# Kernel optimization log

Hardware: AMD Instinct MI355X
Metric: run time of the kernel (lower is better)

Reference implementation:

```python
import jax, jax.numpy as jnp
import numpy as np

C = 1024      # embed dim
NH = 16       # heads
HD = C // NH  # head dim = 64
WS = 14       # window size
MLP_H = 4096  # mlp hidden = 4*C
B, H, W = 16, 28, 28  # batch, token grid (448/16)


def setup_inputs() -> dict:
    key = jax.random.key(0)
    ks = jax.random.split(key, 16)
    s = 0.02
    p = {}
    p["x"] = jax.random.normal(ks[0], (B, H, W, C), jnp.float32)
    p["ln1_w"] = jnp.ones((C,), jnp.float32)
    p["ln1_b"] = jnp.zeros((C,), jnp.float32)
    p["qkv_w"] = jax.random.normal(ks[1], (3 * C, C), jnp.float32) * s
    p["qkv_b"] = jnp.zeros((3 * C,), jnp.float32)
    p["proj_w"] = jax.random.normal(ks[2], (C, C), jnp.float32) * s
    p["proj_b"] = jnp.zeros((C,), jnp.float32)
    p["rel_pos_h"] = jax.random.normal(ks[3], (2 * WS - 1, HD), jnp.float32) * s
    p["rel_pos_w"] = jax.random.normal(ks[4], (2 * WS - 1, HD), jnp.float32) * s
    p["ln2_w"] = jnp.ones((C,), jnp.float32)
    p["ln2_b"] = jnp.zeros((C,), jnp.float32)
    p["fc1_w"] = jax.random.normal(ks[5], (MLP_H, C), jnp.float32) * s
    p["fc1_b"] = jnp.zeros((MLP_H,), jnp.float32)
    p["fc2_w"] = jax.random.normal(ks[6], (C, MLP_H), jnp.float32) * s
    p["fc2_b"] = jnp.zeros((C,), jnp.float32)
    p["conv1_w"] = jax.random.normal(ks[7], (C // 2, C, 1, 1), jnp.float32) * s
    p["n1_w"] = jnp.ones((C // 2,), jnp.float32)
    p["n1_b"] = jnp.zeros((C // 2,), jnp.float32)
    p["conv2_w"] = jax.random.normal(ks[8], (C // 2, C // 2, 3, 3), jnp.float32) * s
    p["n2_w"] = jnp.ones((C // 2,), jnp.float32)
    p["n2_b"] = jnp.zeros((C // 2,), jnp.float32)
    p["conv3_w"] = jax.random.normal(ks[9], (C, C // 2, 1, 1), jnp.float32) * s
    p["n3_w"] = jax.random.normal(ks[10], (C,), jnp.float32) * s
    p["n3_b"] = jnp.zeros((C,), jnp.float32)
    return p


def _ln(x, w, b, eps=1e-5):
    m = x.mean(-1, keepdims=True)
    v = ((x - m) ** 2).mean(-1, keepdims=True)
    return (x - m) * jax.lax.rsqrt(v + eps) * w + b


def _ln_ch(x, w, b, eps=1e-6):
    # detectron2 LayerNorm over channel dim of NCHW
    m = x.mean(1, keepdims=True)
    v = ((x - m) ** 2).mean(1, keepdims=True)
    return (x - m) * jax.lax.rsqrt(v + eps) * w[None, :, None, None] + b[None, :, None, None]


def _win_part(x):
    # [B,H,W,C] -> [B*(H/WS)*(W/WS), WS, WS, C]; 28 is divisible by 14 so no padding
    Bn = x.shape[0]
    x = x.reshape(Bn, H // WS, WS, W // WS, WS, C).transpose(0, 1, 3, 2, 4, 5)
    return x.reshape(-1, WS, WS, C)


def _win_unpart(xw):
    x = xw.reshape(-1, H // WS, W // WS, WS, WS, C).transpose(0, 1, 3, 2, 4, 5)
    return x.reshape(-1, H, W, C)


def _attention(xw, qkv_w, qkv_b, proj_w, proj_b, rel_pos_h, rel_pos_w):
    Bw = xw.shape[0]
    N = WS * WS
    qkv = xw.reshape(Bw, N, C) @ qkv_w.T + qkv_b                       # [Bw,N,3C]
    qkv = qkv.reshape(Bw, N, 3, NH, HD).transpose(2, 3, 0, 1, 4)      # [3,NH,Bw,N,HD]
    q, k, v = qkv.reshape(3, NH * Bw, N, HD)
    attn = (q * HD ** -0.5) @ k.transpose(0, 2, 1)                    # [NH*Bw,N,N]
    # decomposed relative position bias (q_size == k_size == WS)
    idx = jnp.arange(WS)[:, None] - jnp.arange(WS)[None, :] + (WS - 1)
    Rh = rel_pos_h[idx]                                               # [WS,WS,HD]
    Rw = rel_pos_w[idx]
    rq = q.reshape(-1, WS, WS, HD)
    rel_h = jnp.einsum("bhwc,hkc->bhwk", rq, Rh)
    rel_w = jnp.einsum("bhwc,wkc->bhwk", rq, Rw)
    attn = attn.reshape(-1, WS, WS, WS, WS) + rel_h[..., :, None] + rel_w[..., None, :]
    attn = jax.nn.softmax(attn.reshape(NH * Bw, N, N), axis=-1)
    out = attn @ v                                                    # [NH*Bw,N,HD]
    out = out.reshape(NH, Bw, WS, WS, HD).transpose(1, 2, 3, 0, 4).reshape(Bw, WS, WS, C)
    return out @ proj_w.T + proj_b


DN = ("NCHW", "OIHW", "NCHW")


def reference(x, ln1_w, ln1_b, qkv_w, qkv_b, proj_w, proj_b, rel_pos_h, rel_pos_w,
              ln2_w, ln2_b, fc1_w, fc1_b, fc2_w, fc2_b,
              conv1_w, n1_w, n1_b, conv2_w, n2_w, n2_b, conv3_w, n3_w, n3_b):
    shortcut = x
    h = _ln(x, ln1_w, ln1_b)
    h = _win_unpart(_attention(_win_part(h), qkv_w, qkv_b, proj_w, proj_b, rel_pos_h, rel_pos_w))
    x = shortcut + h
    h = _ln(x, ln2_w, ln2_b)
    h = jax.nn.gelu(h @ fc1_w.T + fc1_b, approximate=False)
    x = x + (h @ fc2_w.T + fc2_b)
    # ResBottleneckBlock in NCHW
    y = x.transpose(0, 3, 1, 2)
    r = jax.lax.conv_general_dilated(y, conv1_w, (1, 1), "VALID", dimension_numbers=DN)
    r = jax.nn.gelu(_ln_ch(r, n1_w, n1_b), approximate=False)
    r = jax.lax.conv_general_dilated(r, conv2_w, (1, 1), [(1, 1), (1, 1)], dimension_numbers=DN)
    r = jax.nn.gelu(_ln_ch(r, n2_w, n2_b), approximate=False)
    r = jax.lax.conv_general_dilated(r, conv3_w, (1, 1), "VALID", dimension_numbers=DN)
    r = _ln_ch(r, n3_w, n3_b)
    y = y + r
    return y.transpose(0, 2, 3, 1)
```

## Files before the change

### kernel.cpp

```cpp
#include <hip/hip_runtime.h>
#include <stdint.h>

typedef unsigned short u16;
typedef __attribute__((ext_vector_type(4))) unsigned short u16x4;
typedef __attribute__((ext_vector_type(8))) unsigned short u16x8;
typedef __attribute__((ext_vector_type(8))) __bf16 bf16x8;
typedef __attribute__((ext_vector_type(4))) float f32x4;
typedef __attribute__((ext_vector_type(4))) unsigned int u32x4;

#define TOK 12544
#define CEMB 1024

__device__ __forceinline__ float bf2f(u16 u) {
  union { unsigned int i; float f; } x; x.i = ((unsigned int)u) << 16; return x.f;
}
__device__ __forceinline__ u16 f2bf(float f) {
  union { float f; unsigned int i; } x; x.f = f;
  unsigned int u = x.i;
  u += 0x7fffu + ((u >> 16) & 1u);
  return (u16)(u >> 16);
}
__device__ __forceinline__ float gelu_f(float x) {
  return 0.5f * x * (1.0f + erff(x * 0.7071067811865476f));
}
__device__ __forceinline__ f32x4 mfma_bf16(bf16x8 a, bf16x8 b, f32x4 c) {
  return __builtin_amdgcn_mfma_f32_16x16x32_bf16(a, b, c, 0, 0, 0);
}
__device__ __forceinline__ void glds16(const void* g, void* l) {
  __builtin_amdgcn_global_load_lds(
      (const __attribute__((address_space(1))) void*)g,
      (__attribute__((address_space(3))) void*)l, 16, 0, 0);
}

__global__ __launch_bounds__(256) void zero_k(u32x4* __restrict__ p) {
  u32x4 z = {0u, 0u, 0u, 0u};
  p[threadIdx.x] = z;
}

__global__ __launch_bounds__(256) void cast_bf16_k(const float* __restrict__ in,
                                                   u16* __restrict__ out, int n) {
  int i = (blockIdx.x * 256 + threadIdx.x) * 4;
  if (i >= n) return;
  float4 v = *(const float4*)(in + i);
  u16x4 o = { f2bf(v.x), f2bf(v.y), f2bf(v.z), f2bf(v.w) };
  *(u16x4*)(out + i) = o;
}

__global__ __launch_bounds__(256) void permute_c2_k(const float* __restrict__ in,
                                                    u16* __restrict__ out) {
  int idx = blockIdx.x * 256 + threadIdx.x;
  int o = idx / 4608;
  int rr = idx - o * 4608;
  int pos = rr >> 9;
  int c = rr & 511;
  out[idx] = f2bf(in[(o * 512 + c) * 9 + pos]);
}

template<int COLS, int MODE>
__global__ __launch_bounds__(256)
void ln_k(const float* __restrict__ in, const float* __restrict__ w,
          const float* __restrict__ b, const float* __restrict__ resid,
          u16* __restrict__ outb, float* __restrict__ outf, float eps) {
  int wave = threadIdx.x >> 6, l = threadIdx.x & 63;
  int row = blockIdx.x * 4 + wave;
  const float* x = in + (size_t)row * COLS;
  constexpr int NC = COLS / 256;
  float4 v[NC];
  float s = 0.f, ss = 0.f;
#pragma unroll
  for (int c = 0; c < NC; ++c) {
    v[c] = *(const float4*)(x + (c * 64 + l) * 4);
    s  += v[c].x + v[c].y + v[c].z + v[c].w;
    ss += v[c].x * v[c].x + v[c].y * v[c].y + v[c].z * v[c].z + v[c].w * v[c].w;
  }
#pragma unroll
  for (int off = 32; off; off >>= 1) {
    s  += __shfl_xor(s, off, 64);
    ss += __shfl_xor(ss, off, 64);
  }
  float mean = s * (1.f / COLS);
  float var = ss * (1.f / COLS) - mean * mean;
  float rs = rsqrtf(var + eps);
#pragma unroll
  for (int c = 0; c < NC; ++c) {
    int col = (c * 64 + l) * 4;
    float4 wv = *(const float4*)(w + col);
    float4 bv = *(const float4*)(b + col);
    float o0 = (v[c].x - mean) * rs * wv.x + bv.x;
    float o1 = (v[c].y - mean) * rs * wv.y + bv.y;
    float o2 = (v[c].z - mean) * rs * wv.z + bv.z;
    float o3 = (v[c].w - mean) * rs * wv.w + bv.w;
    if constexpr (MODE == 0) {
      u16x4 o = { f2bf(o0), f2bf(o1), f2bf(o2), f2bf(o3) };
      *(u16x4*)(outb + (size_t)row * COLS + col) = o;
    } else if constexpr (MODE == 1) {
      u16x4 o = { f2bf(gelu_f(o0)), f2bf(gelu_f(o1)), f2bf(gelu_f(o2)), f2bf(gelu_f(o3)) };
      *(u16x4*)(outb + (size_t)row * COLS + col) = o;
    } else {
      float4 rv = *(const float4*)(resid + (size_t)row * COLS + col);
      float4 ov = { rv.x + o0, rv.y + o1, rv.z + o2, rv.w + o3 };
      *(float4*)(outf + (size_t)row * COLS + col) = ov;
    }
  }
}

template<int EPI, bool GATHER>
__global__ __launch_bounds__(256)
void gemm_k(const u16* __restrict__ A, const u16* __restrict__ B,
            int M, int N, int K,
            const float* __restrict__ bias, const float* __restrict__ resid,
            float* __restrict__ outf, u16* __restrict__ outb,
            u16* __restrict__ qg, u16* __restrict__ kg, u16* __restrict__ vg,
            const u16* __restrict__ zeros) {
  __shared__ u16 As[128 * 64];
  __shared__ u16 Bs[128 * 64];
  const int tid = (int)threadIdx.x;
  const int l = tid & 63;
  const int g = l >> 4, r = l & 15;
  const int w = tid >> 6;
  const int wr = w >> 1, wc = w & 1;
  const int rowBase = (int)blockIdx.y * 128;
  const int colBase = (int)blockIdx.x * 128;
  f32x4 acc[4][4] = {};
  const int nk = K >> 6;
  for (int kt = 0; kt < nk; ++kt) {
    __syncthreads();
#pragma unroll
    for (int i = 0; i < 4; ++i) {
      int idx = i * 256 + tid;
      int trow = idx >> 3, tch = idx & 7;
      int tchs = tch ^ (trow & 7);
      const u16* ga;
      if constexpr (!GATHER) {
        ga = A + (size_t)(rowBase + trow) * K + (kt << 6) + (tchs << 3);
      } else {
        int pos = kt >> 3;
        int dy = pos / 3, dx = pos - dy * 3;
        int p = rowBase + trow;
        int bb = p / 784; int rem = p - bb * 784;
        int y = rem / 28; int xx = rem - y * 28;
        int sy = y + dy - 1, sx = xx + dx - 1;
        bool ok = ((unsigned)sy < 28u) && ((unsigned)sx < 28u);
        ga = ok ? (A + (size_t)(bb * 784 + sy * 28 + sx) * 512 + ((kt & 7) << 6) + (tchs << 3))
                : zeros;
      }
      glds16(ga, &As[idx * 8]);
      const u16* gb = B + (size_t)(colBase + trow) * K + (kt << 6) + (tchs << 3);
      glds16(gb, &Bs[idx * 8]);
    }
    __syncthreads();
    bf16x8 af[4][2], bfr[4][2];
#pragma unroll
    for (int m = 0; m < 4; ++m) {
      int rowA = wr * 64 + m * 16 + r;
      int sA = rowA & 7;
      af[m][0] = *(const bf16x8*)&As[rowA * 64 + ((g ^ sA) << 3)];
      af[m][1] = *(const bf16x8*)&As[rowA * 64 + (((g + 4) ^ sA) << 3)];
    }
#pragma unroll
    for (int n = 0; n < 4; ++n) {
      int rowB = wc * 64 + n * 16 + r;
      int sB = rowB & 7;
      bfr[n][0] = *(const bf16x8*)&Bs[rowB * 64 + ((g ^ sB) << 3)];
      bfr[n][1] = *(const bf16x8*)&Bs[rowB * 64 + (((g + 4) ^ sB) << 3)];
    }
#pragma unroll
    for (int m = 0; m < 4; ++m)
#pragma unroll
      for (int n = 0; n < 4; ++n) {
        acc[m][n] = mfma_bf16(af[m][0], bfr[n][0], acc[m][n]);
        acc[m][n] = mfma_bf16(af[m][1], bfr[n][1], acc[m][n]);
      }
  }
#pragma unroll
  for (int m = 0; m < 4; ++m) {
#pragma unroll
    for (int i = 0; i < 4; ++i) {
      int row = rowBase + wr * 64 + m * 16 + g * 4 + i;
#pragma unroll
      for (int n = 0; n < 4; ++n) {
        int col = colBase + wc * 64 + n * 16 + r;
        float v = acc[m][n][i];
        if constexpr (EPI == 0) {
          v += bias[col];
          int bb = row / 784; int rem = row - bb * 784;
          int y = rem / 28; int xx = rem - y * 28;
          int win = bb * 4 + (y / 14) * 2 + (xx / 14);
          int qrow = (y % 14) * 14 + (xx % 14);
          int which = col >> 10; int cid = col & 1023;
          int head = cid >> 6; int d = cid & 63;
          int wh = win * 16 + head;
          u16 bv = f2bf(v);
          if (which == 0)      qg[((size_t)wh * 196 + qrow) * 64 + d] = bv;
          else if (which == 1) kg[((size_t)wh * 196 + qrow) * 64 + d] = bv;
          else                 vg[((size_t)wh * 64 + d) * 224 + qrow] = bv;
        } else if constexpr (EPI == 1) {
          v += bias[col] + resid[(size_t)row * N + col];
          outf[(size_t)row * N + col] = v;
        } else if constexpr (EPI == 2) {
          v = gelu_f(v + bias[col]);
          outb[(size_t)row * N + col] = f2bf(v);
        } else if constexpr (EPI == 3) {
          v += bias[col] + resid[(size_t)row * N + col];
          outf[(size_t)row * N + col] = v;
          outb[(size_t)row * N + col] = f2bf(v);
        } else {
          outf[(size_t)row * N + col] = v;
        }
      }
    }
  }
}

__global__ __launch_bounds__(256)
void rel_k(const u16* __restrict__ qg, const float* __restrict__ rph,
           const float* __restrict__ rpw, float* __restrict__ relh,
           float* __restrict__ relw) {
  int wh = blockIdx.x;
  for (int pair = (int)threadIdx.x; pair < 392; pair += 256) {
    int table = pair >= 196;
    int q = table ? pair - 196 : pair;
    int qi = q / 14, qj = q - qi * 14;
    int qq = table ? qj : qi;
    const u16* qr = qg + ((size_t)wh * 196 + q) * 64;
    float qv[64];
#pragma unroll
    for (int c8 = 0; c8 < 8; ++c8) {
      u16x8 u = *(const u16x8*)(qr + c8 * 8);
#pragma unroll
      for (int j = 0; j < 8; ++j) qv[c8 * 8 + j] = bf2f(u[j]);
    }
    const float* rp = table ? rpw : rph;
    float* out = (table ? relw : relh) + ((size_t)wh * 196 + q) * 14;
    for (int kq = 0; kq < 14; ++kq) {
      const float* rrow = rp + (qq - kq + 13) * 64;
      float sum = 0.f;
#pragma unroll
      for (int c4 = 0; c4 < 16; ++c4) {
        float4 rv = *(const float4*)(rrow + c4 * 4);
        sum += qv[c4 * 4] * rv.x + qv[c4 * 4 + 1] * rv.y +
               qv[c4 * 4 + 2] * rv.z + qv[c4 * 4 + 3] * rv.w;
      }
      out[kq] = sum;
    }
  }
}

__global__ __launch_bounds__(256)
void attn_k(const u16* __restrict__ qg, const u16* __restrict__ kg,
            const u16* __restrict__ vg, const float* __restrict__ relh,
            const float* __restrict__ relw, u16* __restrict__ outb) {
  __shared__ float p_lds[4][32][16];
  __shared__ float o_lds[4][64][17];
  const int wh = blockIdx.x;
  const int tid = (int)threadIdx.x;
  const int w = tid >> 6, l = tid & 63;
  const int g = l >> 4, r = l & 15;
  const int win = wh >> 4, head = wh & 15;
  const size_t qbase = (size_t)wh * 196 * 64;
  const size_t vbase = (size_t)wh * 64 * 224;
  for (int qt = w; qt < 13; qt += 4) {
    int q0 = qt * 16 + r;
    int qc = q0 < 196 ? q0 : 195;
    bf16x8 bq0 = *(const bf16x8*)(qg + qbase + (size_t)qc * 64 + g * 8);
    bf16x8 bq1 = *(const bf16x8*)(qg + qbase + (size_t)qc * 64 + 32 + g * 8);
    f32x4 st[13];
#pragma unroll
    for (int kt = 0; kt < 13; ++kt) {
      int k0 = kt * 16 + r;
      int kc = k0 < 196 ? k0 : 195;
      bf16x8 a0 = *(const bf16x8*)(kg + qbase + (size_t)kc * 64 + g * 8);
      bf16x8 a1 = *(const bf16x8*)(kg + qbase + (size_t)kc * 64 + 32 + g * 8);
      f32x4 z = {0.f, 0.f, 0.f, 0.f};
      z = mfma_bf16(a0, bq0, z);
      z = mfma_bf16(a1, bq1, z);
      st[kt] = z;
    }
    const float* rh = relh + ((size_t)wh * 196 + qc) * 14;
    const float* rw = relw + ((size_t)wh * 196 + qc) * 14;
    float mx = -3.0e38f;
#pragma unroll
    for (int kt = 0; kt < 13; ++kt)
#pragma unroll
      for (int i = 0; i < 4; ++i) {
        int key = kt * 16 + g * 4 + i;
        float sv;
        if (key < 196) {
          int kh = key / 14; int kw = key - kh * 14;
          sv = st[kt][i] * 0.125f + rh[kh] + rw[kw];
        } else sv = -1e30f;
        st[kt][i] = sv;
        mx = fmaxf(mx, sv);
      }
    mx = fmaxf(mx, __shfl_xor(mx, 16, 64));
    mx = fmaxf(mx, __shfl_xor(mx, 32, 64));
    float sum = 0.f;
#pragma unroll
    for (int kt = 0; kt < 13; ++kt)
#pragma unroll
      for (int i = 0; i < 4; ++i) {
        float e = __expf(st[kt][i] - mx);
        st[kt][i] = e;
        sum += e;
      }
    sum += __shfl_xor(sum, 16, 64);
    sum += __shfl_xor(sum, 32, 64);
    float inv = 1.f / sum;
    f32x4 oacc[4] = {};
#pragma unroll
    for (int c = 0; c < 7; ++c) {
#pragma unroll
      for (int f2 = 0; f2 < 2; ++f2) {
        int fi = c * 2 + f2;
#pragma unroll
        for (int i = 0; i < 4; ++i) {
          float pv = (fi < 13) ? st[fi][i] * inv : 0.f;
          p_lds[w][f2 * 16 + g * 4 + i][r] = pv;
        }
      }
      union { u16 u[8]; bf16x8 b; } pu;
#pragma unroll
      for (int j = 0; j < 8; ++j) pu.u[j] = f2bf(p_lds[w][g * 8 + j][r]);
      bf16x8 bp = pu.b;
#pragma unroll
      for (int dt = 0; dt < 4; ++dt) {
        bf16x8 av = *(const bf16x8*)(vg + vbase + (size_t)(dt * 16 + r) * 224 + c * 32 + g * 8);
        oacc[dt] = mfma_bf16(av, bp, oacc[dt]);
      }
    }
#pragma unroll
    for (int dt = 0; dt < 4; ++dt)
#pragma unroll
      for (int i = 0; i < 4; ++i)
        o_lds[w][dt * 16 + g * 4 + i][r] = oacc[dt][i];
    int ql = l >> 2, dseg = l & 3;
    int q = qt * 16 + ql;
    if (q < 196) {
      int qi2 = q / 14, qj2 = q - qi2 * 14;
      int bb = win >> 2; int wy = (win >> 1) & 1; int wx = win & 1;
      int y = wy * 14 + qi2, xx = wx * 14 + qj2;
      size_t tok = (size_t)bb * 784 + y * 28 + xx;
      u16x8 o0, o1;
#pragma unroll
      for (int jj = 0; jj < 8; ++jj) o0[jj] = f2bf(o_lds[w][dseg * 16 + jj][ql]);
#pragma unroll
      for (int jj = 0; jj < 8; ++jj) o1[jj] = f2bf(o_lds[w][dseg * 16 + 8 + jj][ql]);
      *(u16x8*)(outb + tok * 1024 + head * 64 + dseg * 16) = o0;
      *(u16x8*)(outb + tok * 1024 + head * 64 + dseg * 16 + 8) = o1;
    }
  }
}

#define OFF_QKVW  ((size_t)0)
#define OFF_PROJW ((size_t)6291456)
#define OFF_FC1W  ((size_t)8388608)
#define OFF_FC2W  ((size_t)16777216)
#define OFF_C1W   ((size_t)25165824)
#define OFF_C2W   ((size_t)26214400)
#define OFF_C3W   ((size_t)30932992)
#define OFF_ZEROS ((size_t)31981568)
#define OFF_R1    ((size_t)33554432)
#define OFF_QG    (OFF_R1)
#define OFF_KG    ((size_t)59244544)
#define OFF_VG    ((size_t)84934656)
#define OFF_RELH  ((size_t)114294784)
#define OFF_RELW  ((size_t)125534208)
#define OFF_R2    ((size_t)136773632)
#define OFF_R3    ((size_t)162463744)
#define OFF_R4    ((size_t)188153856)
#define OFF_R5    ((size_t)213843968)
#define WS_NEEDED ((size_t)226689024)

extern "C" void kernel_launch(void* const* d_in, const int* in_sizes, int n_in,
                              void* d_out, int out_size, void* d_ws, size_t ws_size,
                              hipStream_t stream) {
  const float* x    = (const float*)d_in[0];
  const float* ln1w = (const float*)d_in[1];
  const float* ln1b = (const float*)d_in[2];
  const float* qkvw = (const float*)d_in[3];
  const float* qkvb = (const float*)d_in[4];
  const float* projw= (const float*)d_in[5];
  const float* projb= (const float*)d_in[6];
  const float* rph  = (const float*)d_in[7];
  const float* rpw  = (const float*)d_in[8];
  const float* ln2w = (const float*)d_in[9];
  const float* ln2b = (const float*)d_in[10];
  const float* fc1w = (const float*)d_in[11];
  const float* fc1b = (const float*)d_in[12];
  const float* fc2w = (const float*)d_in[13];
  const float* fc2b = (const float*)d_in[14];
  const float* c1w  = (const float*)d_in[15];
  const float* n1w  = (const float*)d_in[16];
  const float* n1b  = (const float*)d_in[17];
  const float* c2w  = (const float*)d_in[18];
  const float* n2w  = (const float*)d_in[19];
  const float* n2b  = (const float*)d_in[20];
  const float* c3w  = (const float*)d_in[21];
  const float* n3w  = (const float*)d_in[22];
  const float* n3b  = (const float*)d_in[23];

  if (ws_size < WS_NEEDED) return;

  char* ws = (char*)d_ws;
  u16* qkvw_b = (u16*)(ws + OFF_QKVW);
  u16* projw_b= (u16*)(ws + OFF_PROJW);
  u16* fc1w_b = (u16*)(ws + OFF_FC1W);
  u16* fc2w_b = (u16*)(ws + OFF_FC2W);
  u16* c1w_b  = (u16*)(ws + OFF_C1W);
  u16* c2w_b  = (u16*)(ws + OFF_C2W);
  u16* c3w_b  = (u16*)(ws + OFF_C3W);
  u16* zerosp = (u16*)(ws + OFF_ZEROS);
  u16* qg   = (u16*)(ws + OFF_QG);
  u16* kg   = (u16*)(ws + OFF_KG);
  u16* vg   = (u16*)(ws + OFF_VG);
  float* relh = (float*)(ws + OFF_RELH);
  float* relw = (float*)(ws + OFF_RELW);
  u16* h3   = (u16*)(ws + OFF_R1);
  float* c3f = (float*)(ws + OFF_R1);
  u16* h1   = (u16*)(ws + OFF_R2);
  u16* attnb = (u16*)(ws + OFF_R3);
  u16* h2   = (u16*)(ws + OFF_R3);
  u16* x2b  = (u16*)(ws + OFF_R3);
  float* c1f = (float*)(ws + OFF_R4);
  float* c2f = (float*)(ws + OFF_R4);
  u16* r1   = (u16*)(ws + OFF_R5);
  u16* r2   = (u16*)(ws + OFF_R5);
  float* x1f = (float*)d_out;

  zero_k<<<1, 256, 0, stream>>>((u32x4*)zerosp);
  cast_bf16_k<<<3145728 / 1024, 256, 0, stream>>>(qkvw, qkvw_b, 3145728);
  cast_bf16_k<<<1048576 / 1024, 256, 0, stream>>>(projw, projw_b, 1048576);
  cast_bf16_k<<<4194304 / 1024, 256, 0, stream>>>(fc1w, fc1w_b, 4194304);
  cast_bf16_k<<<4194304 / 1024, 256, 0, stream>>>(fc2w, fc2w_b, 4194304);
  cast_bf16_k<<<524288 / 1024, 256, 0, stream>>>(c1w, c1w_b, 524288);
  cast_bf16_k<<<524288 / 1024, 256, 0, stream>>>(c3w, c3w_b, 524288);
  permute_c2_k<<<2359296 / 256, 256, 0, stream>>>(c2w, c2w_b);

  ln_k<1024, 0><<<TOK / 4, 256, 0, stream>>>(x, ln1w, ln1b, nullptr, h1, nullptr, 1e-5f);
  gemm_k<0, false><<<dim3(3072 / 128, TOK / 128), 256, 0, stream>>>(
      h1, qkvw_b, TOK, 3072, 1024, qkvb, nullptr, nullptr, nullptr, qg, kg, vg, zerosp);
  rel_k<<<1024, 256, 0, stream>>>(qg, rph, rpw, relh, relw);
  attn_k<<<1024, 256, 0, stream>>>(qg, kg, vg, relh, relw, attnb);
  gemm_k<1, false><<<dim3(1024 / 128, TOK / 128), 256, 0, stream>>>(
      attnb, projw_b, TOK, 1024, 1024, projb, x, x1f, nullptr, nullptr, nullptr, nullptr, zerosp);
  ln_k<1024, 0><<<TOK / 4, 256, 0, stream>>>(x1f, ln2w, ln2b, nullptr, h2, nullptr, 1e-5f);
  gemm_k<2, false><<<dim3(4096 / 128, TOK / 128), 256, 0, stream>>>(
      h2, fc1w_b, TOK, 4096, 1024, fc1b, nullptr, nullptr, h3, nullptr, nullptr, nullptr, zerosp);
  gemm_k<3, false><<<dim3(1024 / 128, TOK / 128), 256, 0, stream>>>(
      h3, fc2w_b, TOK, 1024, 4096, fc2b, x1f, x1f, x2b, nullptr, nullptr, nullptr, zerosp);
  gemm_k<4, false><<<dim3(512 / 128, TOK / 128), 256, 0, stream>>>(
      x2b, c1w_b, TOK, 512, 1024, nullptr, nullptr, c1f, nullptr, nullptr, nullptr, nullptr, zerosp);
  ln_k<512, 1><<<TOK / 4, 256, 0, stream>>>(c1f, n1w, n1b, nullptr, r1, nullptr, 1e-6f);
  gemm_k<4, true><<<dim3(512 / 128, TOK / 128), 256, 0, stream>>>(
      r1, c2w_b, TOK, 512, 4608, nullptr, nullptr, c2f, nullptr, nullptr, nullptr, nullptr, zerosp);
  ln_k<512, 1><<<TOK / 4, 256, 0, stream>>>(c2f, n2w, n2b, nullptr, r2, nullptr, 1e-6f);
  gemm_k<4, false><<<dim3(1024 / 128, TOK / 128), 256, 0, stream>>>(
      r2, c3w_b, TOK, 1024, 512, nullptr, nullptr, c3f, nullptr, nullptr, nullptr, nullptr, zerosp);
  ln_k<1024, 2><<<TOK / 4, 256, 0, stream>>>(c3f, n3w, n3b, x1f, nullptr, (float*)d_out, 1e-6f);
}
```

Before: 1.248 ms.

## Stage K/V in LDS for attention and swizzle GEMM block order across XCDs

The attention kernel now loads each window-head's K and V tiles into shared memory once, with an XOR swizzle, using async global-to-LDS copies. The four waves then read K/V from LDS instead of each re-fetching them from global memory. Separately, the GEMM remaps block IDs so that consecutive blocks are spread across the 8 XCDs, aiming for better L2 locality. The larger LDS footprint in attention may reduce occupancy, and the added sched barriers constrain instruction scheduling.

```diff
diff --git a/kernel.cpp b/kernel.cpp
--- a/kernel.cpp
+++ b/kernel.cpp
@@ -119,8 +119,12 @@
   const int g = l >> 4, r = l & 15;
   const int w = tid >> 6;
   const int wr = w >> 1, wc = w & 1;
-  const int rowBase = (int)blockIdx.y * 128;
-  const int colBase = (int)blockIdx.x * 128;
+  const int gx = (int)gridDim.x;
+  const int bid = (int)blockIdx.y * gx + (int)blockIdx.x;
+  const int cpx = (gx * (int)gridDim.y) >> 3;
+  const int swz = (bid & 7) * cpx + (bid >> 3);
+  const int rowBase = (swz / gx) * 128;
+  const int colBase = (swz % gx) * 128;
   f32x4 acc[4][4] = {};
   const int nk = K >> 6;
   for (int kt = 0; kt < nk; ++kt) {
@@ -249,32 +253,56 @@
 __global__ __launch_bounds__(256)
 void attn_k(const u16* __restrict__ qg, const u16* __restrict__ kg,
             const u16* __restrict__ vg, const float* __restrict__ relh,
-            const float* __restrict__ relw, u16* __restrict__ outb) {
-  __shared__ float p_lds[4][32][16];
-  __shared__ float o_lds[4][64][17];
+            const float* __restrict__ relw, u16* __restrict__ outb,
+            const u16* __restrict__ zeros) {
+  __shared__ u16 K_lds[196 * 64];
+  __shared__ u16 V_lds[64 * 256];
+  __shared__ float scr[4][64 * 17];
   const int wh = blockIdx.x;
   const int tid = (int)threadIdx.x;
   const int w = tid >> 6, l = tid & 63;
   const int g = l >> 4, r = l & 15;
   const int win = wh >> 4, head = wh & 15;
-  const size_t qbase = (size_t)wh * 196 * 64;
+  const size_t kbase = (size_t)wh * 196 * 64;
   const size_t vbase = (size_t)wh * 64 * 224;
+#pragma unroll
+  for (int rd = 0; rd < 6; ++rd) {
+    int idx = rd * 256 + tid;
+    int trow = idx >> 3, tch = idx & 7;
+    glds16(kg + kbase + trow * 64 + ((tch ^ (trow & 7)) << 3), &K_lds[idx * 8]);
+  }
+  { int idx = 1536 + tid;
+    if (idx < 1568) {
+      int trow = idx >> 3, tch = idx & 7;
+      glds16(kg + kbase + trow * 64 + ((tch ^ (trow & 7)) << 3), &K_lds[idx * 8]);
+    } }
+#pragma unroll
+  for (int rd = 0; rd < 8; ++rd) {
+    int idx = rd * 256 + tid;
+    int trow = idx >> 5, tch = idx & 31;
+    int tchs = tch ^ (trow & 7);
+    const u16* src = (tchs < 28) ? (vg + vbase + trow * 224 + (tchs << 3)) : zeros;
+    glds16(src, &V_lds[idx * 8]);
+  }
+  __syncthreads();
   for (int qt = w; qt < 13; qt += 4) {
     int q0 = qt * 16 + r;
     int qc = q0 < 196 ? q0 : 195;
-    bf16x8 bq0 = *(const bf16x8*)(qg + qbase + (size_t)qc * 64 + g * 8);
-    bf16x8 bq1 = *(const bf16x8*)(qg + qbase + (size_t)qc * 64 + 32 + g * 8);
+    bf16x8 bq0 = *(const bf16x8*)(qg + kbase + (size_t)qc * 64 + g * 8);
+    bf16x8 bq1 = *(const bf16x8*)(qg + kbase + (size_t)qc * 64 + 32 + g * 8);
     f32x4 st[13];
 #pragma unroll
     for (int kt = 0; kt < 13; ++kt) {
       int k0 = kt * 16 + r;
       int kc = k0 < 196 ? k0 : 195;
-      bf16x8 a0 = *(const bf16x8*)(kg + qbase + (size_t)kc * 64 + g * 8);
-      bf16x8 a1 = *(const bf16x8*)(kg + qbase + (size_t)kc * 64 + 32 + g * 8);
+      int sk = kc & 7;
+      bf16x8 a0 = *(const bf16x8*)&K_lds[kc * 64 + ((g ^ sk) << 3)];
+      bf16x8 a1 = *(const bf16x8*)&K_lds[kc * 64 + (((g + 4) ^ sk) << 3)];
       f32x4 z = {0.f, 0.f, 0.f, 0.f};
       z = mfma_bf16(a0, bq0, z);
       z = mfma_bf16(a1, bq1, z);
       st[kt] = z;
+      __builtin_amdgcn_sched_barrier(0);
     }
     const float* rh = relh + ((size_t)wh * 196 + qc) * 14;
     const float* rw = relw + ((size_t)wh * 196 + qc) * 14;
@@ -315,24 +343,27 @@
 #pragma unroll
         for (int i = 0; i < 4; ++i) {
           float pv = (fi < 13) ? st[fi][i] * inv : 0.f;
-          p_lds[w][f2 * 16 + g * 4 + i][r] = pv;
+          scr[w][(f2 * 16 + g * 4 + i) * 16 + r] = pv;
         }
       }
       union { u16 u[8]; bf16x8 b; } pu;
 #pragma unroll
-      for (int j = 0; j < 8; ++j) pu.u[j] = f2bf(p_lds[w][g * 8 + j][r]);
+      for (int j = 0; j < 8; ++j) pu.u[j] = f2bf(scr[w][(g * 8 + j) * 16 + r]);
       bf16x8 bp = pu.b;
 #pragma unroll
       for (int dt = 0; dt < 4; ++dt) {
-        bf16x8 av = *(const bf16x8*)(vg + vbase + (size_t)(dt * 16 + r) * 224 + c * 32 + g * 8);
+        int vr = dt * 16 + r;
+        int cc = c * 4 + g;
+        bf16x8 av = *(const bf16x8*)&V_lds[vr * 256 + ((cc ^ (vr & 7)) << 3)];
         oacc[dt] = mfma_bf16(av, bp, oacc[dt]);
       }
+      __builtin_amdgcn_sched_barrier(0);
     }
 #pragma unroll
     for (int dt = 0; dt < 4; ++dt)
 #pragma unroll
       for (int i = 0; i < 4; ++i)
-        o_lds[w][dt * 16 + g * 4 + i][r] = oacc[dt][i];
+        scr[w][(dt * 16 + g * 4 + i) * 17 + r] = oacc[dt][i];
     int ql = l >> 2, dseg = l & 3;
     int q = qt * 16 + ql;
     if (q < 196) {
@@ -342,9 +373,9 @@
       size_t tok = (size_t)bb * 784 + y * 28 + xx;
       u16x8 o0, o1;
 #pragma unroll
-      for (int jj = 0; jj < 8; ++jj) o0[jj] = f2bf(o_lds[w][dseg * 16 + jj][ql]);
-#pragma unroll
-      for (int jj = 0; jj < 8; ++jj) o1[jj] = f2bf(o_lds[w][dseg * 16 + 8 + jj][ql]);
+      for (int jj = 0; jj < 8; ++jj) o0[jj] = f2bf(scr[w][(dseg * 16 + jj) * 17 + ql]);
+#pragma unroll
+      for (int jj = 0; jj < 8; ++jj) o1[jj] = f2bf(scr[w][(dseg * 16 + 8 + jj) * 17 + ql]);
       *(u16x8*)(outb + tok * 1024 + head * 64 + dseg * 16) = o0;
       *(u16x8*)(outb + tok * 1024 + head * 64 + dseg * 16 + 8) = o1;
     }
@@ -440,7 +471,7 @@
   gemm_k<0, false><<<dim3(3072 / 128, TOK / 128), 256, 0, stream>>>(
       h1, qkvw_b, TOK, 3072, 1024, qkvb, nullptr, nullptr, nullptr, qg, kg, vg, zerosp);
   rel_k<<<1024, 256, 0, stream>>>(qg, rph, rpw, relh, relw);
-  attn_k<<<1024, 256, 0, stream>>>(qg, kg, vg, relh, relw, attnb);
+  attn_k<<<1024, 256, 0, stream>>>(qg, kg, vg, relh, relw, attnb, zerosp);
   gemm_k<1, false><<<dim3(1024 / 128, TOK / 128), 256, 0, stream>>>(
       attnb, projw_b, TOK, 1024, 1024, projb, x, x1f, nullptr, nullptr, nullptr, nullptr, zerosp);
   ln_k<1024, 0><<<TOK / 4, 256, 0, stream>>>(x1f, ln2w, ln2b, nullptr, h2, nullptr, 1e-5f);
```

Result: faster. 1.208 ms (-3.2%).
